# Kernel optimization log

Measured on AMD Instinct MI355X. Metric: run time of the kernel, lower is better.

Reference implementation:

```python
import jax, jax.numpy as jnp
import numpy as np

NY, NU, NH = 64, 32, 512
NHRZ, B = 2048, 128


def setup_inputs() -> dict:
    key = jax.random.key(0)
    ks = jax.random.split(key, 8)
    # PyTorch-default-like scale: 1/sqrt(fan_in) keeps the long recurrence stable.
    s_y2x = 1.0 / np.sqrt(NY)
    s_xu2x = 1.0 / np.sqrt(NH + NU)
    s_x2y = 1.0 / np.sqrt(NH)
    return {
        "y0": jax.random.normal(ks[0], (B, NY), jnp.float32),
        "U": jax.random.normal(ks[1], (NHRZ, B, NU), jnp.float32),
        "y2x_w": jax.random.normal(ks[2], (NH, NY), jnp.float32) * s_y2x,
        "y2x_b": jax.random.normal(ks[3], (NH,), jnp.float32) * s_y2x,
        "xu2x_w": jax.random.normal(ks[4], (NH, NH + NU), jnp.float32) * s_xu2x,
        "xu2x_b": jax.random.normal(ks[5], (NH,), jnp.float32) * s_xu2x,
        "x2y_w": jax.random.normal(ks[6], (NY, NH), jnp.float32) * s_x2y,
        "x2y_b": jax.random.normal(ks[7], (NY,), jnp.float32) * s_x2y,
    }


def reference(y0, U, y2x_w, y2x_b, xu2x_w, xu2x_b, x2y_w, x2y_b):
    x0 = y0 @ y2x_w.T + y2x_b  # [B, NH]
    # x_{k+1} = A x_k + Bm u_k + b  (cat((x,u)) @ W.T == x @ A.T + u @ Bm.T)
    A = xu2x_w[:, :NH].T      # [NH, NH]
    Bm = xu2x_w[:, NH:].T     # [NU, NH]

    def step(x, u):
        xn = x @ A + u @ Bm + xu2x_b
        return xn, xn

    _, Xs = jax.lax.scan(step, x0, U)          # [NHRZ, B, NH]
    X = jnp.concatenate([x0[None], Xs], axis=0)  # [NHRZ+1, B, NH]
    Y = X @ x2y_w.T + x2y_b                      # [NHRZ+1, B, NY]
    return Y
```

## Files before the change

kernel.cpp:

```cpp
#include <hip/hip_runtime.h>


#define T_CH 64

typedef _Float16 h8 __attribute__((ext_vector_type(8)));
typedef float    f4 __attribute__((ext_vector_type(4)));

__device__ __forceinline__ f4 MFMA16(h8 a, h8 b, f4 c) {
  return __builtin_amdgcn_mfma_f32_16x16x32_f16(a, b, c, 0, 0, 0);
}
__device__ __forceinline__ int xoff(int row, int bc) {
  return row * 1024 + (bc ^ ((row & 7) << 4));
}
__device__ __forceinline__ size_t PK512(int tn, int kb, int ln) {
  return ((size_t)(tn * 64 + kb) * 16 + ln) * 8;
}

__global__ __launch_bounds__(256) void k_prep(
    const float* __restrict__ xw, const float* __restrict__ yw,
    const float* __restrict__ xub,
    _Float16* __restrict__ A_pk, _Float16* __restrict__ A_rm,
    _Float16* __restrict__ SWpk, _Float16* __restrict__ R_rm,
    _Float16* __restrict__ Wst_pk) {
  int tid = blockIdx.x * 256 + threadIdx.x;
  if (tid < 32768) {
    int g = tid; int ln = g & 15, kb = (g >> 4) & 63, tn = g >> 10;
    const float* s = xw + (tn * 16 + ln) * 544 + kb * 8;
    _Float16* d = A_pk + (size_t)g * 8;
#pragma unroll
    for (int j = 0; j < 8; j++) d[j] = (_Float16)s[j];
  } else if (tid < 65536) {
    int g = tid - 32768; int k = g >> 6, n8 = (g & 63) * 8;
#pragma unroll
    for (int j = 0; j < 8; j++) A_rm[(size_t)k * 512 + n8 + j] = (_Float16)xw[(size_t)(n8 + j) * 544 + k];
  } else if (tid < 69632) {
    int g = tid - 65536; int ln = g & 15, kb = (g >> 4) & 63, tn = g >> 10;
    const float* s = yw + (tn * 16 + ln) * 512 + kb * 8;
    _Float16* d = SWpk + (size_t)g * 8;
#pragma unroll
    for (int j = 0; j < 8; j++) d[j] = (_Float16)s[j];
  } else if (tid < 72704) {
    int g = tid - 69632; int row = g >> 6, n8 = (g & 63) * 8;
#pragma unroll
    for (int j = 0; j < 8; j++) {
      float v = 0.f;
      if (row < 32) v = xw[(size_t)(n8 + j) * 544 + 512 + row];
      else if (row == 32) v = xub[n8 + j];
      R_rm[(size_t)row * 512 + n8 + j] = (_Float16)v;
    }
  } else if (tid < 74752) {
    int g = tid - 72704; int ln = g & 15, gg = (g >> 4) & 3, tn = g >> 6;
    _Float16* d = Wst_pk + (size_t)g * 8;
#pragma unroll
    for (int j = 0; j < 8; j++) d[j] = (_Float16)xw[(size_t)(tn * 16 + ln) * 544 + 512 + gg * 8 + j];
  }
}

__global__ __launch_bounds__(256) void k_x0(
    const float* __restrict__ y0, const float* __restrict__ w,
    const float* __restrict__ b, _Float16* __restrict__ x0h) {
  int tid = blockIdx.x * 256 + threadIdx.x;
  int bb = tid >> 9, h = tid & 511;
  float acc = b[h];
  const float* wr = w + h * 64;
  const float* yr = y0 + bb * 64;
#pragma unroll 8
  for (int i = 0; i < 64; i++) acc += yr[i] * wr[i];
  x0h[(size_t)bb * 512 + h] = (_Float16)acc;
}

__global__ __launch_bounds__(256) void k_chain(
    const _Float16* __restrict__ rm_in, const _Float16* __restrict__ pk_in,
    _Float16* __restrict__ rm_out, _Float16* __restrict__ pk_out,
    _Float16* __restrict__ R_rm, _Float16* __restrict__ Wst_pk,
    _Float16* __restrict__ SWpk, int nR, int nSW, int off) {
  const int bid = blockIdx.x;
  const int tid = threadIdx.x;
  const int w = tid >> 6, ln = tid & 15, g = (tid >> 4) & 3;
  if (bid < 64) {
    int Mb = (bid >> 3) * 64, Nb = (bid & 7) * 64;
    int mrow = Mb + w * 16 + ln;
    f4 acc[4];
#pragma unroll
    for (int i = 0; i < 4; i++) { f4 z = {0.f, 0.f, 0.f, 0.f}; acc[i] = z; }
    for (int k0 = 0; k0 < 512; k0 += 32) {
      h8 af = *(const h8*)(rm_in + (size_t)mrow * 512 + k0 + g * 8);
#pragma unroll
      for (int i = 0; i < 4; i++) {
        h8 bf = *(const h8*)(pk_in + PK512((Nb >> 4) + i, (k0 >> 3) + g, ln));
        acc[i] = MFMA16(af, bf, acc[i]);
      }
    }
    int mr0 = Mb + w * 16 + g * 4;
#pragma unroll
    for (int i = 0; i < 4; i++) {
      int n = Nb + i * 16 + ln;
#pragma unroll
      for (int r = 0; r < 4; r++) rm_out[(size_t)(mr0 + r) * 512 + n] = (_Float16)acc[i][r];
      _Float16* pd = pk_out + (size_t)((n >> 4) * 64 + (mr0 >> 3)) * 128 + (n & 15) * 8 + (mr0 & 7);
#pragma unroll
      for (int r = 0; r < 4; r++) pd[r] = (_Float16)acc[i][r];
    }
  } else if (bid < 64 + nR) {
    const int k = bid - 64;
    const _Float16* src = R_rm + (size_t)k * 24576;
    _Float16* dst = R_rm + (size_t)(k + off) * 24576;
    _Float16* wpk = Wst_pk + (size_t)(k + off) * 16384;
    f4 acc[3][8];
#pragma unroll
    for (int mt = 0; mt < 3; mt++)
#pragma unroll
      for (int i = 0; i < 8; i++) { f4 z = {0.f, 0.f, 0.f, 0.f}; acc[mt][i] = z; }
    for (int k0 = 0; k0 < 512; k0 += 32) {
      h8 af[3];
#pragma unroll
      for (int mt = 0; mt < 3; mt++)
        af[mt] = *(const h8*)(src + (size_t)(mt * 16 + ln) * 512 + k0 + g * 8);
#pragma unroll
      for (int i = 0; i < 8; i++) {
        h8 bf = *(const h8*)(pk_in + PK512(w * 8 + i, (k0 >> 3) + g, ln));
#pragma unroll
        for (int mt = 0; mt < 3; mt++) acc[mt][i] = MFMA16(af[mt], bf, acc[mt][i]);
      }
    }
#pragma unroll
    for (int mt = 0; mt < 3; mt++)
#pragma unroll
      for (int i = 0; i < 8; i++) {
        int tn = w * 8 + i, col = tn * 16 + ln;
        int r0 = mt * 16 + g * 4;
#pragma unroll
        for (int r = 0; r < 4; r++) dst[(size_t)(r0 + r) * 512 + col] = (_Float16)acc[mt][i][r];
        if (mt < 2) {
          _Float16* pd = wpk + ((size_t)(tn * 4 + (r0 >> 3)) * 16 + ln) * 8 + (r0 & 7);
#pragma unroll
          for (int r = 0; r < 4; r++) pd[r] = (_Float16)acc[mt][i][r];
        }
      }
  } else {
    const int q = bid - 64 - nR;
    const int t = q >> 3, mb = q & 7;
    const _Float16* src = SWpk + (size_t)t * 32768;
    _Float16* dst = SWpk + (size_t)(t + off) * 32768;
    f4 acc[4];
#pragma unroll
    for (int c = 0; c < 4; c++) { f4 z = {0.f, 0.f, 0.f, 0.f}; acc[c] = z; }
    const int rbase = mb * 64 + w * 16;
    for (int k0 = 0; k0 < 512; k0 += 32) {
      h8 af = *(const h8*)(rm_in + (size_t)(rbase + ln) * 512 + k0 + g * 8);
#pragma unroll
      for (int c = 0; c < 4; c++) {
        h8 bf = *(const h8*)(src + PK512(c, (k0 >> 3) + g, ln));
        acc[c] = MFMA16(af, bf, acc[c]);
      }
    }
    const int r0 = rbase + g * 4;
#pragma unroll
    for (int c = 0; c < 4; c++) {
      _Float16* pd = dst + ((size_t)(c * 64 + (r0 >> 3)) * 16 + ln) * 8 + (r0 & 7);
#pragma unroll
      for (int r = 0; r < 4; r++) pd[r] = (_Float16)acc[c][r];
    }
  }
}

__global__ __launch_bounds__(256) void k_gk(
    const _Float16* __restrict__ R_rm, const _Float16* __restrict__ SWpk0,
    _Float16* __restrict__ Gpk) {
  const int tap = blockIdx.x;
  const int tid = threadIdx.x;
  const int w = tid >> 6, ln = tid & 15, g = (tid >> 4) & 3;
  const int mt = w & 1, cb = (w >> 1) * 2;
  const _Float16* src = R_rm + (size_t)tap * 24576;
  f4 acc[2];
#pragma unroll
  for (int c = 0; c < 2; c++) { f4 z = {0.f, 0.f, 0.f, 0.f}; acc[c] = z; }
  for (int k0 = 0; k0 < 512; k0 += 32) {
    h8 af = *(const h8*)(src + (size_t)(mt * 16 + ln) * 512 + k0 + g * 8);
#pragma unroll
    for (int c = 0; c < 2; c++) {
      h8 bf = *(const h8*)(SWpk0 + PK512(cb + c, (k0 >> 3) + g, ln));
      acc[c] = MFMA16(af, bf, acc[c]);
    }
  }
  const int r0 = mt * 16 + g * 4;
#pragma unroll
  for (int c = 0; c < 2; c++) {
    _Float16* pd = Gpk + (size_t)tap * 2048 + ((size_t)((cb + c) * 4 + (r0 >> 3)) * 16 + ln) * 8 + (r0 & 7);
#pragma unroll
    for (int r = 0; r < 4; r++) pd[r] = (_Float16)acc[c][r];
  }
}

__global__ __launch_bounds__(256) void k_misc(
    const _Float16* __restrict__ R_rm, const float* __restrict__ yw,
    const float* __restrict__ yb, float* __restrict__ ybias,
    float* __restrict__ bias32) {
  __shared__ float gb[2048];
  const int tid = threadIdx.x;
  for (int idx = tid; idx < 2048; idx += 256) {
    int i = idx >> 6, c = idx & 63;
    const _Float16* br = R_rm + (size_t)i * 24576 + 32 * 512;
    const float* wc = yw + c * 512;
    float s = 0.f;
#pragma unroll 8
    for (int h = 0; h < 512; h++) s += (float)br[h] * wc[h];
    gb[idx] = s;
  }
  __syncthreads();
  for (int idx = tid; idx < 2048; idx += 256) {
    int t = (idx >> 6) + 1, c = idx & 63;
    float s = yb[c];
    for (int i = 0; i < t; i++) s += gb[i * 64 + c];
    ybias[t * 64 + c] = s;
  }
  for (int n = tid; n < 512; n += 256) {
    float s = 0.f;
#pragma unroll
    for (int i = 0; i < 32; i++) s += (float)R_rm[(size_t)i * 24576 + 32 * 512 + n];
    bias32[n] = s;
  }
}

__global__ __launch_bounds__(512) void k_y0(
    const _Float16* __restrict__ x0h, const _Float16* __restrict__ SWpk0,
    const float* __restrict__ yb, float* __restrict__ Y) {
  const int tid = threadIdx.x;
  const int w = tid >> 6, ln = tid & 15, g = (tid >> 4) & 3;
  f4 acc[4];
#pragma unroll
  for (int c = 0; c < 4; c++) { f4 z = {0.f, 0.f, 0.f, 0.f}; acc[c] = z; }
  for (int k0 = 0; k0 < 512; k0 += 32) {
    h8 af = *(const h8*)(x0h + (size_t)(w * 16 + ln) * 512 + k0 + g * 8);
#pragma unroll
    for (int c = 0; c < 4; c++) {
      h8 bf = *(const h8*)(SWpk0 + PK512(c, (k0 >> 3) + g, ln));
      acc[c] = MFMA16(af, bf, acc[c]);
    }
  }
#pragma unroll
  for (int c = 0; c < 4; c++) {
    int col = c * 16 + ln;
#pragma unroll
    for (int r = 0; r < 4; r++)
      Y[(size_t)(w * 16 + g * 4 + r) * 64 + col] = acc[c][r] + yb[col];
  }
}

__global__ __launch_bounds__(512) void k_p1(
    const float* __restrict__ U, const _Float16* __restrict__ Wst_pk,
    const _Float16* __restrict__ x0h, const _Float16* __restrict__ A32_pk,
    const float* __restrict__ bias32, _Float16* __restrict__ Zh) {
  const int rb = blockIdx.x, j = blockIdx.y;
  const int row0 = rb * 32;
  const int tid = threadIdx.x;
  const int w = tid >> 6, ln = tid & 15, g = (tid >> 4) & 3;
  f4 acc[2][4];
#pragma unroll
  for (int tm = 0; tm < 2; tm++)
#pragma unroll
    for (int i = 0; i < 4; i++) { f4 z = {0.f, 0.f, 0.f, 0.f}; acc[tm][i] = z; }
#pragma unroll 4
  for (int t = 0; t < 32; t++) {
    const _Float16* wp = Wst_pk + (size_t)(31 - t) * 16384;
    h8 uf[2];
#pragma unroll
    for (int tm = 0; tm < 2; tm++) {
      const float* up = U + ((size_t)(j * 32 + t) * 128 + row0 + tm * 16 + ln) * 32 + g * 8;
      const float4 ua = *(const float4*)up;
      const float4 ub = *(const float4*)(up + 4);
      h8 v;
      v[0] = (_Float16)ua.x; v[1] = (_Float16)ua.y; v[2] = (_Float16)ua.z; v[3] = (_Float16)ua.w;
      v[4] = (_Float16)ub.x; v[5] = (_Float16)ub.y; v[6] = (_Float16)ub.z; v[7] = (_Float16)ub.w;
      uf[tm] = v;
    }
#pragma unroll
    for (int i = 0; i < 4; i++) {
      h8 bf = *(const h8*)(wp + ((size_t)((w * 4 + i) * 4 + g) * 16 + ln) * 8);
#pragma unroll
      for (int tm = 0; tm < 2; tm++) acc[tm][i] = MFMA16(uf[tm], bf, acc[tm][i]);
    }
  }
  if (j == 0) {
    for (int k0 = 0; k0 < 512; k0 += 32) {
      h8 af[2];
#pragma unroll
      for (int tm = 0; tm < 2; tm++)
        af[tm] = *(const h8*)(x0h + (size_t)(row0 + tm * 16 + ln) * 512 + k0 + g * 8);
#pragma unroll
      for (int i = 0; i < 4; i++) {
        h8 bf = *(const h8*)(A32_pk + PK512(w * 4 + i, (k0 >> 3) + g, ln));
#pragma unroll
        for (int tm = 0; tm < 2; tm++) acc[tm][i] = MFMA16(af[tm], bf, acc[tm][i]);
      }
    }
  }
#pragma unroll
  for (int tm = 0; tm < 2; tm++)
#pragma unroll
    for (int i = 0; i < 4; i++) {
      const int n = (w * 4 + i) * 16 + ln;
      const float bz = bias32[n];
#pragma unroll
      for (int r = 0; r < 4; r++) {
        const int mr = tm * 16 + g * 4 + r;
        Zh[((size_t)j * 128 + row0 + mr) * 512 + n] = (_Float16)(acc[tm][i][r] + bz);
      }
    }
}

__global__ __launch_bounds__(512) void k_scan(
    const _Float16* __restrict__ Zin, _Float16* __restrict__ Zout,
    const _Float16* __restrict__ P_pk, int d) {
  extern __shared__ char smem[];
  const int rb = blockIdx.x, j = blockIdx.y;
  const int row0 = rb * 16;
  const int tid = threadIdx.x;
  if (j < d) {
    const uint4* s = (const uint4*)(Zin + ((size_t)j * 128 + row0) * 512);
    uint4* dst = (uint4*)(Zout + ((size_t)j * 128 + row0) * 512);
#pragma unroll
    for (int q = 0; q < 2; q++) dst[tid + q * 512] = s[tid + q * 512];
    return;
  }
  const int w = tid >> 6, ln = tid & 15, g = (tid >> 4) & 3;
  {
    const int row = tid >> 5;
    const int c = (tid & 31) * 16;
    const _Float16* s = Zin + ((size_t)(j - d) * 128 + row0 + row) * 512 + c;
#pragma unroll
    for (int q = 0; q < 2; q++)
      *(h8*)(smem + xoff(row, 2 * (c + q * 8))) = *(const h8*)(s + q * 8);
  }
  __syncthreads();
  f4 acc[4];
#pragma unroll
  for (int i = 0; i < 4; i++) {
    const int n = (w * 4 + i) * 16 + ln;
#pragma unroll
    for (int r = 0; r < 4; r++)
      acc[i][r] = (float)Zin[((size_t)j * 128 + row0 + g * 4 + r) * 512 + n];
  }
#pragma unroll 4
  for (int k0 = 0; k0 < 512; k0 += 32) {
    h8 xa = *(const h8*)(smem + xoff(ln, 2 * k0 + 16 * g));
#pragma unroll
    for (int i = 0; i < 4; i++) {
      h8 bf = *(const h8*)(P_pk + PK512(w * 4 + i, (k0 >> 3) + g, ln));
      acc[i] = MFMA16(xa, bf, acc[i]);
    }
  }
#pragma unroll
  for (int i = 0; i < 4; i++) {
    const int n = (w * 4 + i) * 16 + ln;
#pragma unroll
    for (int r = 0; r < 4; r++)
      Zout[((size_t)j * 128 + row0 + g * 4 + r) * 512 + n] = (_Float16)acc[i][r];
  }
}

__global__ __launch_bounds__(512) void k_p2(
    const float* __restrict__ U, const _Float16* __restrict__ Zh,
    const _Float16* __restrict__ x0h, const _Float16* __restrict__ SWpk,
    const _Float16* __restrict__ Gpk, const float* __restrict__ ybias,
    float* __restrict__ Y) {
  const int nb = blockIdx.x, j = blockIdx.y;
  const int tid = threadIdx.x;
  const int w = tid >> 6, ln = tid & 15, g = (tid >> 4) & 3;
  const int mh = w >> 2;
  const int tw = nb * 4 + (w & 3) + 1;
  const _Float16* S = (j == 0) ? x0h : (Zh + (size_t)(j - 1) * 65536);
  const _Float16* SW = SWpk + (size_t)tw * 32768;
  f4 acc[4][4];
#pragma unroll
  for (int mt = 0; mt < 4; mt++)
#pragma unroll
    for (int c = 0; c < 4; c++) { f4 z = {0.f, 0.f, 0.f, 0.f}; acc[mt][c] = z; }
  for (int k0 = 0; k0 < 512; k0 += 32) {
    h8 af[4];
#pragma unroll
    for (int mt = 0; mt < 4; mt++)
      af[mt] = *(const h8*)(S + (size_t)(mh * 64 + mt * 16 + ln) * 512 + k0 + g * 8);
#pragma unroll
    for (int c = 0; c < 4; c++) {
      h8 bf = *(const h8*)(SW + PK512(c, (k0 >> 3) + g, ln));
#pragma unroll
      for (int mt = 0; mt < 4; mt++) acc[mt][c] = MFMA16(af[mt], bf, acc[mt][c]);
    }
  }
#pragma unroll 4
  for (int i = 0; i < tw; i++) {
    h8 uf[4];
#pragma unroll
    for (int mt = 0; mt < 4; mt++) {
      const float* up = U + ((size_t)(j * 32 + i) * 128 + mh * 64 + mt * 16 + ln) * 32 + g * 8;
      const float4 ua = *(const float4*)up;
      const float4 ub = *(const float4*)(up + 4);
      h8 v;
      v[0] = (_Float16)ua.x; v[1] = (_Float16)ua.y; v[2] = (_Float16)ua.z; v[3] = (_Float16)ua.w;
      v[4] = (_Float16)ub.x; v[5] = (_Float16)ub.y; v[6] = (_Float16)ub.z; v[7] = (_Float16)ub.w;
      uf[mt] = v;
    }
    const _Float16* gp = Gpk + (size_t)(tw - 1 - i) * 2048;
#pragma unroll
    for (int c = 0; c < 4; c++) {
      h8 bf = *(const h8*)(gp + ((size_t)(c * 4 + g) * 16 + ln) * 8);
#pragma unroll
      for (int mt = 0; mt < 4; mt++) acc[mt][c] = MFMA16(uf[mt], bf, acc[mt][c]);
    }
  }
  const size_t ybase = (size_t)(j * 32 + tw) * 128;
#pragma unroll
  for (int mt = 0; mt < 4; mt++)
#pragma unroll
    for (int c = 0; c < 4; c++) {
      const int col = c * 16 + ln;
      const float yv = ybias[tw * 64 + col];
#pragma unroll
      for (int r = 0; r < 4; r++) {
        const int row = mh * 64 + mt * 16 + g * 4 + r;
        Y[(ybase + row) * 64 + col] = acc[mt][c][r] + yv;
      }
    }
}

extern "C" void kernel_launch(void* const* d_in, const int* in_sizes, int n_in,
                              void* d_out, int out_size, void* d_ws, size_t ws_size,
                              hipStream_t stream) {
  const float* y0   = (const float*)d_in[0];
  const float* U    = (const float*)d_in[1];
  const float* y2xw = (const float*)d_in[2];
  const float* y2xb = (const float*)d_in[3];
  const float* xw   = (const float*)d_in[4];
  const float* xub  = (const float*)d_in[5];
  const float* x2yw = (const float*)d_in[6];
  const float* x2yb = (const float*)d_in[7];
  float* Y = (float*)d_out;
  char* ws = (char*)d_ws;

  _Float16* A_rm  = (_Float16*)(ws + 0x000000);
  _Float16* A_pk  = (_Float16*)(ws + 0x080000);
  auto rm = [&](int m) { return (_Float16*)(ws + 0x100000 + (size_t)(m - 1) * 0x80000); };
  auto pkL = [&](int m) { return (_Float16*)(ws + 0x480000 + (size_t)(m - 1) * 0x80000); };
  _Float16* R_rm  = (_Float16*)(ws + 0x680000);
  _Float16* Z2    = (_Float16*)(ws + 0x000000);
  _Float16* Zh    = (_Float16*)(ws + 0x800000);
  auto pkH = [&](int m) { return (_Float16*)(ws + 0x1000000 + (size_t)(m - 5) * 0x80000); };
  _Float16* Wst_pk = (_Float16*)(ws + 0x1200000);
  _Float16* SWpk   = (_Float16*)(ws + 0x1300000);
  _Float16* Gpk    = (_Float16*)(ws + 0x1510000);
  float*    ybias  = (float*)   (ws + 0x1530000);
  float*    bias32 = (float*)   (ws + 0x1534000);
  _Float16* x0h    = (_Float16*)(ws + 0x1538000);
  auto pw_rm = [&](int m) { return m == 0 ? A_rm : rm(m); };
  auto pw_pk = [&](int m) { return m == 0 ? A_pk : (m <= 4 ? pkL(m) : pkH(m)); };

  k_prep<<<292, 256, 0, stream>>>(xw, x2yw, xub, A_pk, A_rm, SWpk, R_rm, Wst_pk);
  k_x0<<<256, 256, 0, stream>>>(y0, y2xw, y2xb, x0h);
  for (int m = 0; m < 8; m++) {
    int nR = (m <= 4) ? (1 << m) : 0;
    int nSW = (m <= 4) ? (1 << m) : (m == 5 ? 1 : 0);
    int off = (m == 5) ? 32 : (1 << m);
    _Float16* rmo = (m == 7) ? rm(1) : rm(m + 1);
    k_chain<<<64 + nR + 8 * nSW, 256, 0, stream>>>(
        pw_rm(m), pw_pk(m), rmo, pw_pk(m + 1), R_rm, Wst_pk, SWpk, nR, nSW, off);
  }
  k_gk<<<32, 256, 0, stream>>>(R_rm, SWpk, Gpk);
  k_misc<<<1, 256, 0, stream>>>(R_rm, x2yw, x2yb, ybias, bias32);
  k_y0<<<1, 512, 0, stream>>>(x0h, SWpk, x2yb, Y);
  k_p1<<<dim3(4, T_CH), 512, 0, stream>>>(U, Wst_pk, x0h, pkH(5), bias32, Zh);
  k_scan<<<dim3(8, T_CH), 512, 16384, stream>>>(Zh, Z2, pkH(5), 1);
  k_scan<<<dim3(8, T_CH), 512, 16384, stream>>>(Z2, Zh, pkH(6), 2);
  k_scan<<<dim3(8, T_CH), 512, 16384, stream>>>(Zh, Z2, pkH(7), 4);
  k_scan<<<dim3(8, T_CH), 512, 16384, stream>>>(Z2, Zh, pkH(8), 8);
  k_p2<<<dim3(8, T_CH), 512, 0, stream>>>(U, Zh, x0h, SWpk, Gpk, ybias, Y);
}
```

Baseline: 639.3 us.

## Fuse small setup kernels, retile chain GEMM, and load-balance output projection

Merges k_prep and k_x0 into one launch, and k_gk, k_misc and k_y0 into one multi-role k_aux launch, which removes several small launch gaps. The chain power GEMM moves from 64 blocks to 256 blocks with 32x32 tiles so more CUs work on each squaring step. k_p2 now pairs time offsets ta and 33-ta in each block so the triangular U-convolution work is balanced across 1024 blocks. Smaller tiles mean less B-fragment reuse per block, and k_aux keeps the serial single-block bias computation.

Result: faster. 608.4 us (-4.8%).

```diff
diff --git a/kernel.cpp b/kernel.cpp
--- a/kernel.cpp
+++ b/kernel.cpp
@@ -16,12 +16,13 @@
   return ((size_t)(tn * 64 + kb) * 16 + ln) * 8;
 }
 
-__global__ __launch_bounds__(256) void k_prep(
+__global__ __launch_bounds__(256) void k_prep0(
     const float* __restrict__ xw, const float* __restrict__ yw,
-    const float* __restrict__ xub,
+    const float* __restrict__ xub, const float* __restrict__ y0,
+    const float* __restrict__ y2xw, const float* __restrict__ y2xb,
     _Float16* __restrict__ A_pk, _Float16* __restrict__ A_rm,
     _Float16* __restrict__ SWpk, _Float16* __restrict__ R_rm,
-    _Float16* __restrict__ Wst_pk) {
+    _Float16* __restrict__ Wst_pk, _Float16* __restrict__ x0h) {
   int tid = blockIdx.x * 256 + threadIdx.x;
   if (tid < 32768) {
     int g = tid; int ln = g & 15, kb = (g >> 4) & 63, tn = g >> 10;
@@ -53,20 +54,16 @@
     _Float16* d = Wst_pk + (size_t)g * 8;
 #pragma unroll
     for (int j = 0; j < 8; j++) d[j] = (_Float16)xw[(size_t)(tn * 16 + ln) * 544 + 512 + gg * 8 + j];
-  }
-}
-
-__global__ __launch_bounds__(256) void k_x0(
-    const float* __restrict__ y0, const float* __restrict__ w,
-    const float* __restrict__ b, _Float16* __restrict__ x0h) {
-  int tid = blockIdx.x * 256 + threadIdx.x;
-  int bb = tid >> 9, h = tid & 511;
-  float acc = b[h];
-  const float* wr = w + h * 64;
-  const float* yr = y0 + bb * 64;
+  } else if (tid < 140288) {
+    int id = tid - 74752;
+    int bb = id >> 9, h = id & 511;
+    float acc = y2xb[h];
+    const float* wr = y2xw + h * 64;
+    const float* yr = y0 + bb * 64;
 #pragma unroll 8
-  for (int i = 0; i < 64; i++) acc += yr[i] * wr[i];
-  x0h[(size_t)bb * 512 + h] = (_Float16)acc;
+    for (int i = 0; i < 64; i++) acc += yr[i] * wr[i];
+    x0h[(size_t)bb * 512 + h] = (_Float16)acc;
+  }
 }
 
 __global__ __launch_bounds__(256) void k_chain(
@@ -77,32 +74,25 @@
   const int bid = blockIdx.x;
   const int tid = threadIdx.x;
   const int w = tid >> 6, ln = tid & 15, g = (tid >> 4) & 3;
-  if (bid < 64) {
-    int Mb = (bid >> 3) * 64, Nb = (bid & 7) * 64;
-    int mrow = Mb + w * 16 + ln;
-    f4 acc[4];
-#pragma unroll
-    for (int i = 0; i < 4; i++) { f4 z = {0.f, 0.f, 0.f, 0.f}; acc[i] = z; }
+  if (bid < 256) {
+    const int Mb = (bid >> 4) * 32, Nb = (bid & 15) * 32;
+    const int mt = w >> 1, nt = w & 1;
+    const int mrow = Mb + mt * 16 + ln;
+    f4 acc = {0.f, 0.f, 0.f, 0.f};
     for (int k0 = 0; k0 < 512; k0 += 32) {
       h8 af = *(const h8*)(rm_in + (size_t)mrow * 512 + k0 + g * 8);
-#pragma unroll
-      for (int i = 0; i < 4; i++) {
-        h8 bf = *(const h8*)(pk_in + PK512((Nb >> 4) + i, (k0 >> 3) + g, ln));
-        acc[i] = MFMA16(af, bf, acc[i]);
-      }
-    }
-    int mr0 = Mb + w * 16 + g * 4;
-#pragma unroll
-    for (int i = 0; i < 4; i++) {
-      int n = Nb + i * 16 + ln;
-#pragma unroll
-      for (int r = 0; r < 4; r++) rm_out[(size_t)(mr0 + r) * 512 + n] = (_Float16)acc[i][r];
-      _Float16* pd = pk_out + (size_t)((n >> 4) * 64 + (mr0 >> 3)) * 128 + (n & 15) * 8 + (mr0 & 7);
-#pragma unroll
-      for (int r = 0; r < 4; r++) pd[r] = (_Float16)acc[i][r];
-    }
-  } else if (bid < 64 + nR) {
-    const int k = bid - 64;
+      h8 bf = *(const h8*)(pk_in + PK512((Nb >> 4) + nt, (k0 >> 3) + g, ln));
+      acc = MFMA16(af, bf, acc);
+    }
+    const int mr0 = Mb + mt * 16 + g * 4;
+    const int n = Nb + nt * 16 + ln;
+#pragma unroll
+    for (int r = 0; r < 4; r++) rm_out[(size_t)(mr0 + r) * 512 + n] = (_Float16)acc[r];
+    _Float16* pd = pk_out + (size_t)((n >> 4) * 64 + (mr0 >> 3)) * 128 + (n & 15) * 8 + (mr0 & 7);
+#pragma unroll
+    for (int r = 0; r < 4; r++) pd[r] = (_Float16)acc[r];
+  } else if (bid < 256 + nR) {
+    const int k = bid - 256;
     const _Float16* src = R_rm + (size_t)k * 24576;
     _Float16* dst = R_rm + (size_t)(k + off) * 24576;
     _Float16* wpk = Wst_pk + (size_t)(k + off) * 16384;
@@ -138,7 +128,7 @@
         }
       }
   } else {
-    const int q = bid - 64 - nR;
+    const int q = bid - 256 - nR;
     const int t = q >> 3, mb = q & 7;
     const _Float16* src = SWpk + (size_t)t * 32768;
     _Float16* dst = SWpk + (size_t)(t + off) * 32768;
@@ -164,86 +154,82 @@
   }
 }
 
-__global__ __launch_bounds__(256) void k_gk(
+__global__ __launch_bounds__(512) void k_aux(
     const _Float16* __restrict__ R_rm, const _Float16* __restrict__ SWpk0,
-    _Float16* __restrict__ Gpk) {
-  const int tap = blockIdx.x;
+    _Float16* __restrict__ Gpk, const float* __restrict__ yw,
+    const float* __restrict__ yb, float* __restrict__ ybias,
+    float* __restrict__ bias32, const _Float16* __restrict__ x0h,
+    float* __restrict__ Y) {
+  __shared__ float gb[2048];
+  const int bid = blockIdx.x;
   const int tid = threadIdx.x;
-  const int w = tid >> 6, ln = tid & 15, g = (tid >> 4) & 3;
-  const int mt = w & 1, cb = (w >> 1) * 2;
-  const _Float16* src = R_rm + (size_t)tap * 24576;
-  f4 acc[2];
-#pragma unroll
-  for (int c = 0; c < 2; c++) { f4 z = {0.f, 0.f, 0.f, 0.f}; acc[c] = z; }
-  for (int k0 = 0; k0 < 512; k0 += 32) {
-    h8 af = *(const h8*)(src + (size_t)(mt * 16 + ln) * 512 + k0 + g * 8);
-#pragma unroll
-    for (int c = 0; c < 2; c++) {
-      h8 bf = *(const h8*)(SWpk0 + PK512(cb + c, (k0 >> 3) + g, ln));
-      acc[c] = MFMA16(af, bf, acc[c]);
-    }
-  }
-  const int r0 = mt * 16 + g * 4;
-#pragma unroll
-  for (int c = 0; c < 2; c++) {
-    _Float16* pd = Gpk + (size_t)tap * 2048 + ((size_t)((cb + c) * 4 + (r0 >> 3)) * 16 + ln) * 8 + (r0 & 7);
-#pragma unroll
-    for (int r = 0; r < 4; r++) pd[r] = (_Float16)acc[c][r];
-  }
-}
-
-__global__ __launch_bounds__(256) void k_misc(
-    const _Float16* __restrict__ R_rm, const float* __restrict__ yw,
-    const float* __restrict__ yb, float* __restrict__ ybias,
-    float* __restrict__ bias32) {
-  __shared__ float gb[2048];
-  const int tid = threadIdx.x;
-  for (int idx = tid; idx < 2048; idx += 256) {
-    int i = idx >> 6, c = idx & 63;
-    const _Float16* br = R_rm + (size_t)i * 24576 + 32 * 512;
-    const float* wc = yw + c * 512;
-    float s = 0.f;
+  if (bid < 32) {
+    if (tid < 256) {
+      const int w = tid >> 6, ln = tid & 15, g = (tid >> 4) & 3;
+      const int mt = w & 1, cb = (w >> 1) * 2;
+      const _Float16* src = R_rm + (size_t)bid * 24576;
+      f4 acc[2];
+#pragma unroll
+      for (int c = 0; c < 2; c++) { f4 z = {0.f, 0.f, 0.f, 0.f}; acc[c] = z; }
+      for (int k0 = 0; k0 < 512; k0 += 32) {
+        h8 af = *(const h8*)(src + (size_t)(mt * 16 + ln) * 512 + k0 + g * 8);
+#pragma unroll
+        for (int c = 0; c < 2; c++) {
+          h8 bf = *(const h8*)(SWpk0 + PK512(cb + c, (k0 >> 3) + g, ln));
+          acc[c] = MFMA16(af, bf, acc[c]);
+        }
+      }
+      const int r0 = mt * 16 + g * 4;
+#pragma unroll
+      for (int c = 0; c < 2; c++) {
+        _Float16* pd = Gpk + (size_t)bid * 2048 + ((size_t)((cb + c) * 4 + (r0 >> 3)) * 16 + ln) * 8 + (r0 & 7);
+#pragma unroll
+        for (int r = 0; r < 4; r++) pd[r] = (_Float16)acc[c][r];
+      }
+    }
+  } else if (bid == 32) {
+    for (int idx = tid; idx < 2048; idx += 512) {
+      int i = idx >> 6, c = idx & 63;
+      const _Float16* br = R_rm + (size_t)i * 24576 + 32 * 512;
+      const float* wc = yw + c * 512;
+      float s = 0.f;
 #pragma unroll 8
-    for (int h = 0; h < 512; h++) s += (float)br[h] * wc[h];
-    gb[idx] = s;
-  }
-  __syncthreads();
-  for (int idx = tid; idx < 2048; idx += 256) {
-    int t = (idx >> 6) + 1, c = idx & 63;
-    float s = yb[c];
-    for (int i = 0; i < t; i++) s += gb[i * 64 + c];
-    ybias[t * 64 + c] = s;
-  }
-  for (int n = tid; n < 512; n += 256) {
-    float s = 0.f;
-#pragma unroll
-    for (int i = 0; i < 32; i++) s += (float)R_rm[(size_t)i * 24576 + 32 * 512 + n];
-    bias32[n] = s;
-  }
-}
-
-__global__ __launch_bounds__(512) void k_y0(
-    const _Float16* __restrict__ x0h, const _Float16* __restrict__ SWpk0,
-    const float* __restrict__ yb, float* __restrict__ Y) {
-  const int tid = threadIdx.x;
-  const int w = tid >> 6, ln = tid & 15, g = (tid >> 4) & 3;
-  f4 acc[4];
-#pragma unroll
-  for (int c = 0; c < 4; c++) { f4 z = {0.f, 0.f, 0.f, 0.f}; acc[c] = z; }
-  for (int k0 = 0; k0 < 512; k0 += 32) {
-    h8 af = *(const h8*)(x0h + (size_t)(w * 16 + ln) * 512 + k0 + g * 8);
+      for (int h = 0; h < 512; h++) s += (float)br[h] * wc[h];
+      gb[idx] = s;
+    }
+    __syncthreads();
+    for (int idx = tid; idx < 2048; idx += 512) {
+      int t = (idx >> 6) + 1, c = idx & 63;
+      float s = yb[c];
+      for (int i = 0; i < t; i++) s += gb[i * 64 + c];
+      ybias[t * 64 + c] = s;
+    }
+    for (int n = tid; n < 512; n += 512) {
+      float s = 0.f;
+#pragma unroll
+      for (int i = 0; i < 32; i++) s += (float)R_rm[(size_t)i * 24576 + 32 * 512 + n];
+      bias32[n] = s;
+    }
+  } else {
+    const int w = tid >> 6, ln = tid & 15, g = (tid >> 4) & 3;
+    f4 acc[4];
+#pragma unroll
+    for (int c = 0; c < 4; c++) { f4 z = {0.f, 0.f, 0.f, 0.f}; acc[c] = z; }
+    for (int k0 = 0; k0 < 512; k0 += 32) {
+      h8 af = *(const h8*)(x0h + (size_t)(w * 16 + ln) * 512 + k0 + g * 8);
+#pragma unroll
+      for (int c = 0; c < 4; c++) {
+        h8 bf = *(const h8*)(SWpk0 + PK512(c, (k0 >> 3) + g, ln));
+        acc[c] = MFMA16(af, bf, acc[c]);
+      }
+    }
 #pragma unroll
     for (int c = 0; c < 4; c++) {
-      h8 bf = *(const h8*)(SWpk0 + PK512(c, (k0 >> 3) + g, ln));
-      acc[c] = MFMA16(af, bf, acc[c]);
-    }
-  }
-#pragma unroll
-  for (int c = 0; c < 4; c++) {
-    int col = c * 16 + ln;
-#pragma unroll
-    for (int r = 0; r < 4; r++)
-      Y[(size_t)(w * 16 + g * 4 + r) * 64 + col] = acc[c][r] + yb[col];
+      int col = c * 16 + ln;
+#pragma unroll
+      for (int r = 0; r < 4; r++)
+        Y[(size_t)(w * 16 + g * 4 + r) * 64 + col] = acc[c][r] + yb[col];
+    }
   }
 }
 
@@ -364,64 +350,75 @@
     const _Float16* __restrict__ x0h, const _Float16* __restrict__ SWpk,
     const _Float16* __restrict__ Gpk, const float* __restrict__ ybias,
     float* __restrict__ Y) {
-  const int nb = blockIdx.x, j = blockIdx.y;
+  const int b = blockIdx.x;
+  const int r = b >> 3;
+  const int j = (b & 7) * 8 + (r >> 4);
+  const int ta = (r & 15) + 1, tb = 33 - ta;
   const int tid = threadIdx.x;
   const int w = tid >> 6, ln = tid & 15, g = (tid >> 4) & 3;
-  const int mh = w >> 2;
-  const int tw = nb * 4 + (w & 3) + 1;
+  const int row = w * 16 + ln;
   const _Float16* S = (j == 0) ? x0h : (Zh + (size_t)(j - 1) * 65536);
-  const _Float16* SW = SWpk + (size_t)tw * 32768;
-  f4 acc[4][4];
-#pragma unroll
-  for (int mt = 0; mt < 4; mt++)
-#pragma unroll
-    for (int c = 0; c < 4; c++) { f4 z = {0.f, 0.f, 0.f, 0.f}; acc[mt][c] = z; }
+  const _Float16* SWa = SWpk + (size_t)ta * 32768;
+  const _Float16* SWb = SWpk + (size_t)tb * 32768;
+  f4 acc[2][4];
+#pragma unroll
+  for (int th = 0; th < 2; th++)
+#pragma unroll
+    for (int c = 0; c < 4; c++) { f4 z = {0.f, 0.f, 0.f, 0.f}; acc[th][c] = z; }
+#pragma unroll 4
   for (int k0 = 0; k0 < 512; k0 += 32) {
-    h8 af[4];
-#pragma unroll
-    for (int mt = 0; mt < 4; mt++)
-      af[mt] = *(const h8*)(S + (size_t)(mh * 64 + mt * 16 + ln) * 512 + k0 + g * 8);
+    h8 af = *(const h8*)(S + (size_t)row * 512 + k0 + g * 8);
 #pragma unroll
     for (int c = 0; c < 4; c++) {
-      h8 bf = *(const h8*)(SW + PK512(c, (k0 >> 3) + g, ln));
-#pragma unroll
-      for (int mt = 0; mt < 4; mt++) acc[mt][c] = MFMA16(af[mt], bf, acc[mt][c]);
-    }
-  }
-#pragma unroll 4
-  for (int i = 0; i < tw; i++) {
-    h8 uf[4];
-#pragma unroll
-    for (int mt = 0; mt < 4; mt++) {
-      const float* up = U + ((size_t)(j * 32 + i) * 128 + mh * 64 + mt * 16 + ln) * 32 + g * 8;
-      const float4 ua = *(const float4*)up;
-      const float4 ub = *(const float4*)(up + 4);
-      h8 v;
-      v[0] = (_Float16)ua.x; v[1] = (_Float16)ua.y; v[2] = (_Float16)ua.z; v[3] = (_Float16)ua.w;
-      v[4] = (_Float16)ub.x; v[5] = (_Float16)ub.y; v[6] = (_Float16)ub.z; v[7] = (_Float16)ub.w;
-      uf[mt] = v;
-    }
-    const _Float16* gp = Gpk + (size_t)(tw - 1 - i) * 2048;
+      h8 b0 = *(const h8*)(SWa + PK512(c, (k0 >> 3) + g, ln));
+      acc[0][c] = MFMA16(af, b0, acc[0][c]);
+      h8 b1 = *(const h8*)(SWb + PK512(c, (k0 >> 3) + g, ln));
+      acc[1][c] = MFMA16(af, b1, acc[1][c]);
+    }
+  }
+  const size_t ubase = ((size_t)(j * 32) * 128 + row) * 32 + g * 8;
+#pragma unroll 2
+  for (int i = 0; i < ta; ++i) {
+    const float* up = U + ubase + (size_t)i * 4096;
+    const float4 ua = *(const float4*)up;
+    const float4 ub = *(const float4*)(up + 4);
+    h8 af;
+    af[0] = (_Float16)ua.x; af[1] = (_Float16)ua.y; af[2] = (_Float16)ua.z; af[3] = (_Float16)ua.w;
+    af[4] = (_Float16)ub.x; af[5] = (_Float16)ub.y; af[6] = (_Float16)ub.z; af[7] = (_Float16)ub.w;
+    const _Float16* ga = Gpk + (size_t)(ta - 1 - i) * 2048;
+    const _Float16* gbp = Gpk + (size_t)(tb - 1 - i) * 2048;
 #pragma unroll
     for (int c = 0; c < 4; c++) {
-      h8 bf = *(const h8*)(gp + ((size_t)(c * 4 + g) * 16 + ln) * 8);
-#pragma unroll
-      for (int mt = 0; mt < 4; mt++) acc[mt][c] = MFMA16(uf[mt], bf, acc[mt][c]);
-    }
-  }
-  const size_t ybase = (size_t)(j * 32 + tw) * 128;
-#pragma unroll
-  for (int mt = 0; mt < 4; mt++)
+      acc[0][c] = MFMA16(af, *(const h8*)(ga + ((size_t)(c * 4 + g) * 16 + ln) * 8), acc[0][c]);
+      acc[1][c] = MFMA16(af, *(const h8*)(gbp + ((size_t)(c * 4 + g) * 16 + ln) * 8), acc[1][c]);
+    }
+  }
+#pragma unroll 2
+  for (int i = ta; i < tb; ++i) {
+    const float* up = U + ubase + (size_t)i * 4096;
+    const float4 ua = *(const float4*)up;
+    const float4 ub = *(const float4*)(up + 4);
+    h8 af;
+    af[0] = (_Float16)ua.x; af[1] = (_Float16)ua.y; af[2] = (_Float16)ua.z; af[3] = (_Float16)ua.w;
+    af[4] = (_Float16)ub.x; af[5] = (_Float16)ub.y; af[6] = (_Float16)ub.z; af[7] = (_Float16)ub.w;
+    const _Float16* gbp = Gpk + (size_t)(tb - 1 - i) * 2048;
+#pragma unroll
+    for (int c = 0; c < 4; c++)
+      acc[1][c] = MFMA16(af, *(const h8*)(gbp + ((size_t)(c * 4 + g) * 16 + ln) * 8), acc[1][c]);
+  }
+#pragma unroll
+  for (int th = 0; th < 2; th++) {
+    const int tw = th ? tb : ta;
+    const size_t ybase = (size_t)(j * 32 + tw) * 128;
 #pragma unroll
     for (int c = 0; c < 4; c++) {
       const int col = c * 16 + ln;
       const float yv = ybias[tw * 64 + col];
 #pragma unroll
-      for (int r = 0; r < 4; r++) {
-        const int row = mh * 64 + mt * 16 + g * 4 + r;
-        Y[(ybase + row) * 64 + col] = acc[mt][c][r] + yv;
-      }
-    }
+      for (int rr = 0; rr < 4; rr++)
+        Y[(ybase + w * 16 + g * 4 + rr) * 64 + col] = acc[th][c][rr] + yv;
+    }
+  }
 }
 
 extern "C" void kernel_launch(void* const* d_in, const int* in_sizes, int n_in,
@@ -455,23 +452,21 @@
   auto pw_rm = [&](int m) { return m == 0 ? A_rm : rm(m); };
   auto pw_pk = [&](int m) { return m == 0 ? A_pk : (m <= 4 ? pkL(m) : pkH(m)); };
 
-  k_prep<<<292, 256, 0, stream>>>(xw, x2yw, xub, A_pk, A_rm, SWpk, R_rm, Wst_pk);
-  k_x0<<<256, 256, 0, stream>>>(y0, y2xw, y2xb, x0h);
+  k_prep0<<<548, 256, 0, stream>>>(xw, x2yw, xub, y0, y2xw, y2xb,
+                                   A_pk, A_rm, SWpk, R_rm, Wst_pk, x0h);
   for (int m = 0; m < 8; m++) {
     int nR = (m <= 4) ? (1 << m) : 0;
     int nSW = (m <= 4) ? (1 << m) : (m == 5 ? 1 : 0);
     int off = (m == 5) ? 32 : (1 << m);
     _Float16* rmo = (m == 7) ? rm(1) : rm(m + 1);
-    k_chain<<<64 + nR + 8 * nSW, 256, 0, stream>>>(
+    k_chain<<<256 + nR + 8 * nSW, 256, 0, stream>>>(
         pw_rm(m), pw_pk(m), rmo, pw_pk(m + 1), R_rm, Wst_pk, SWpk, nR, nSW, off);
   }
-  k_gk<<<32, 256, 0, stream>>>(R_rm, SWpk, Gpk);
-  k_misc<<<1, 256, 0, stream>>>(R_rm, x2yw, x2yb, ybias, bias32);
-  k_y0<<<1, 512, 0, stream>>>(x0h, SWpk, x2yb, Y);
+  k_aux<<<34, 512, 0, stream>>>(R_rm, SWpk, Gpk, x2yw, x2yb, ybias, bias32, x0h, Y);
   k_p1<<<dim3(4, T_CH), 512, 0, stream>>>(U, Wst_pk, x0h, pkH(5), bias32, Zh);
   k_scan<<<dim3(8, T_CH), 512, 16384, stream>>>(Zh, Z2, pkH(5), 1);
   k_scan<<<dim3(8, T_CH), 512, 16384, stream>>>(Z2, Zh, pkH(6), 2);
   k_scan<<<dim3(8, T_CH), 512, 16384, stream>>>(Zh, Z2, pkH(7), 4);
   k_scan<<<dim3(8, T_CH), 512, 16384, stream>>>(Z2, Zh, pkH(8), 8);
-  k_p2<<<dim3(8, T_CH), 512, 0, stream>>>(U, Zh, x0h, SWpk, Gpk, ybias, Y);
-}
+  k_p2<<<1024, 512, 0, stream>>>(U, Zh, x0h, SWpk, Gpk, ybias, Y);
+}
```
